# Optimization experiments

Hardware: AMD Instinct MI355X
Metric: run time of the kernel (lower is better)

Reference implementation:

```python
import jax, jax.numpy as jnp
import numpy as np
import math

B, D, K = 16384, 512, 16384  # batch, feature_dim, codebook_size
H, Z = D // 2, D // 4        # encoder hidden (256), code dim (128)
LN_EPS = 1e-5


def _layernorm(x, gamma, beta):
    mu = x.mean(axis=-1, keepdims=True)
    var = ((x - mu) ** 2).mean(axis=-1, keepdims=True)
    return (x - mu) * jax.lax.rsqrt(var + LN_EPS) * gamma + beta


def setup_inputs() -> dict:
    key = jax.random.key(0)
    ks = jax.random.split(key, 8)
    def lin(k, fan_in, fan_out):
        bound = 1.0 / math.sqrt(fan_in)
        kw, kb = jax.random.split(k)
        W = jax.random.uniform(kw, (fan_in, fan_out), jnp.float32, -bound, bound)
        b = jax.random.uniform(kb, (fan_out,), jnp.float32, -bound, bound)
        return W, b
    W1, b1 = lin(ks[0], D, H)
    W2, b2 = lin(ks[1], H, Z)
    W3, b3 = lin(ks[2], Z, H)
    W4, b4 = lin(ks[3], H, D)
    return {
        "features": jax.random.normal(ks[4], (B, D), jnp.float32),
        "W1": W1, "b1": b1,
        "g1": jnp.ones((H,), jnp.float32), "be1": jnp.zeros((H,), jnp.float32),
        "W2": W2, "b2": b2,
        "codebook": jax.random.normal(ks[5], (K, Z), jnp.float32) * 0.1,
        "W3": W3, "b3": b3,
        "g2": jnp.ones((H,), jnp.float32), "be2": jnp.zeros((H,), jnp.float32),
        "W4": W4, "b4": b4,
    }


def reference(features, W1, b1, g1, be1, W2, b2, codebook, W3, b3, g2, be2, W4, b4):
    # encoder: Linear -> LayerNorm -> GELU -> Linear
    h = jax.nn.gelu(_layernorm(features @ W1 + b1, g1, be1), approximate=False)
    encoded = h @ W2 + b2                                    # [B, Z]
    d2 = (jnp.sum(encoded ** 2, axis=-1, keepdims=True)
          + jnp.sum(codebook ** 2, axis=-1)[None, :]
          - 2.0 * encoded @ codebook.T)                      # [B, K]
    distances = jnp.sqrt(jnp.maximum(d2, 0.0))
    quantized_indices = jnp.argmin(distances, axis=-1)       # [B]
    quantized = codebook[quantized_indices]                  # [B, Z]
    # decoder: Linear -> LayerNorm -> GELU -> Linear
    dh = jax.nn.gelu(_layernorm(quantized @ W3 + b3, g2, be2), approximate=False)
    reconstructed = dh @ W4 + b4                             # [B, D]
    reconstruction_error = jnp.mean((reconstructed - features) ** 2, axis=-1)  # [B]
    # MDL bit estimates
    index_bits = math.log2(K)
    scale = reconstruction_error.mean() + 1e-8
    log_prob = -jnp.abs(reconstruction_error) / scale - jnp.log(2.0 * scale)
    error_bits = -log_prob / math.log(2.0)
    total_bits = index_bits + error_bits                     # [B]
    compression_ratio = D * 32.0 / total_bits                # [B]
    return (reconstruction_error, compression_ratio, total_bits, quantized_indices)
```

## Files before the change

### kernel.cpp

```cpp
#include <hip/hip_runtime.h>
#include <math.h>

#define BN 16384
#define DN 512
#define KN 16384
#define HN 256
#define ZN 128

#define EPS_G 0.04f

typedef _Float16 f16x8 __attribute__((ext_vector_type(8)));
typedef _Float16 f16x4 __attribute__((ext_vector_type(4)));
typedef float f32x4 __attribute__((ext_vector_type(4)));

__device__ __forceinline__ unsigned sortkey(float v) {
    unsigned u = __float_as_uint(v);
    return u ^ (0x80000000u | (unsigned)((int)u >> 31));
}
__device__ __forceinline__ float unsortf(unsigned s) {
    unsigned u = (s & 0x80000000u) ? (s ^ 0x80000000u) : ~s;
    return __uint_as_float(u);
}
__device__ __forceinline__ unsigned umin2(unsigned a, unsigned b) { return a < b ? a : b; }
__device__ __forceinline__ unsigned umax2(unsigned a, unsigned b) { return a > b ? a : b; }

__global__ __launch_bounds__(256) void wtrans_kernel(
    const float* __restrict__ W1, const float* __restrict__ W2,
    const float* __restrict__ W3, const float* __restrict__ W4,
    float* __restrict__ Wp1, float* __restrict__ Wp2,
    float* __restrict__ Wp3, float* __restrict__ Wp4)
{
    const int g = blockIdx.x * 256 + threadIdx.x;
    if (g < 131072) {
        const int k = g >> 8, j = g & 255;
        Wp1[((size_t)k * 64 + (j & 63)) * 4 + (j >> 6)] = W1[g];
    } else if (g < 262144) {
        const int i = g - 131072;
        const int k = i >> 9, d = i & 511;
        Wp4[((size_t)k * 128 + (d & 127)) * 4 + (d >> 7)] = W4[i];
    } else if (g < 294912) {
        const int i = g - 262144;
        const int k = i >> 7, j = i & 127;
        Wp2[((size_t)k * 32 + (j & 31)) * 4 + (j >> 5)] = W2[i];
    } else {
        const int i = g - 294912;
        const int k = i >> 8, j = i & 255;
        Wp3[((size_t)k * 64 + (j & 63)) * 4 + (j >> 6)] = W3[i];
    }
}

__global__ __launch_bounds__(256) void enc_kernel(
    const float* __restrict__ feat, const float* __restrict__ Wp1, const float* __restrict__ b1,
    const float* __restrict__ g1, const float* __restrict__ be1,
    const float* __restrict__ Wp2, const float* __restrict__ b2,
    float* __restrict__ encoded, _Float16* __restrict__ xh, _Float16* __restrict__ xl)
{
    __shared__ float xf[16][512];
    __shared__ float hb[16][256];
    const int tid = threadIdx.x;
    const int rbase = blockIdx.x * 16;

    {
        const float4* src = (const float4*)(feat + (size_t)rbase * 512);
        float4* dst = (float4*)&xf[0][0];
        #pragma unroll
        for (int i = 0; i < 8; ++i) dst[tid * 8 + i] = src[tid * 8 + i];
    }
    __syncthreads();

    const int j0 = tid & 63, rg = tid >> 6;
    float acc[4][4];
    #pragma unroll
    for (int c = 0; c < 4; ++c) {
        float bv = b1[c * 64 + j0];
        #pragma unroll
        for (int r = 0; r < 4; ++r) acc[r][c] = bv;
    }
    for (int k = 0; k < 512; k += 4) {
        f32x4 wv[4];
        #pragma unroll
        for (int kk = 0; kk < 4; ++kk)
            wv[kk] = *(const f32x4*)(Wp1 + ((size_t)(k + kk) * 64 + j0) * 4);
        f32x4 xv[4];
        #pragma unroll
        for (int r = 0; r < 4; ++r) xv[r] = *(const f32x4*)&xf[rg * 4 + r][k];
        #pragma unroll
        for (int r = 0; r < 4; ++r)
            #pragma unroll
            for (int c = 0; c < 4; ++c) {
                acc[r][c] = fmaf(xv[r][0], wv[0][c], acc[r][c]);
                acc[r][c] = fmaf(xv[r][1], wv[1][c], acc[r][c]);
                acc[r][c] = fmaf(xv[r][2], wv[2][c], acc[r][c]);
                acc[r][c] = fmaf(xv[r][3], wv[3][c], acc[r][c]);
            }
    }

    float s1[4], s2[4];
    #pragma unroll
    for (int r = 0; r < 4; ++r) {
        s1[r] = acc[r][0] + acc[r][1] + acc[r][2] + acc[r][3];
        s2[r] = acc[r][0] * acc[r][0] + acc[r][1] * acc[r][1]
              + acc[r][2] * acc[r][2] + acc[r][3] * acc[r][3];
    }
    #pragma unroll
    for (int m = 1; m < 64; m <<= 1) {
        #pragma unroll
        for (int r = 0; r < 4; ++r) {
            s1[r] += __shfl_xor(s1[r], m, 64);
            s2[r] += __shfl_xor(s2[r], m, 64);
        }
    }
    {
        float gvv[4], bvv[4];
        #pragma unroll
        for (int c = 0; c < 4; ++c) { gvv[c] = g1[c * 64 + j0]; bvv[c] = be1[c * 64 + j0]; }
        #pragma unroll
        for (int r = 0; r < 4; ++r) {
            float mu = s1[r] * (1.0f / 256.0f);
            float var = fmaxf(s2[r] * (1.0f / 256.0f) - mu * mu, 0.0f);
            float rstd = rsqrtf(var + 1e-5f);
            #pragma unroll
            for (int c = 0; c < 4; ++c) {
                float t = (acc[r][c] - mu) * rstd * gvv[c] + bvv[c];
                hb[rg * 4 + r][c * 64 + j0] = 0.5f * t * (1.0f + erff(t * 0.70710678118654752f));
            }
        }
    }
    __syncthreads();

    const int j02 = tid & 31, rg2 = tid >> 5;
    float a2[2][4];
    #pragma unroll
    for (int c = 0; c < 4; ++c) {
        float bv = b2[c * 32 + j02];
        #pragma unroll
        for (int r = 0; r < 2; ++r) a2[r][c] = bv;
    }
    for (int k = 0; k < 256; k += 4) {
        f32x4 wv[4];
        #pragma unroll
        for (int kk = 0; kk < 4; ++kk)
            wv[kk] = *(const f32x4*)(Wp2 + ((size_t)(k + kk) * 32 + j02) * 4);
        f32x4 hv[2];
        #pragma unroll
        for (int r = 0; r < 2; ++r) hv[r] = *(const f32x4*)&hb[rg2 * 2 + r][k];
        #pragma unroll
        for (int r = 0; r < 2; ++r)
            #pragma unroll
            for (int c = 0; c < 4; ++c) {
                a2[r][c] = fmaf(hv[r][0], wv[0][c], a2[r][c]);
                a2[r][c] = fmaf(hv[r][1], wv[1][c], a2[r][c]);
                a2[r][c] = fmaf(hv[r][2], wv[2][c], a2[r][c]);
                a2[r][c] = fmaf(hv[r][3], wv[3][c], a2[r][c]);
            }
    }
    #pragma unroll
    for (int r = 0; r < 2; ++r) {
        const size_t row = rbase + rg2 * 2 + r;
        #pragma unroll
        for (int c = 0; c < 4; ++c) {
            const size_t idx = row * 128 + c * 32 + j02;
            const float v = a2[r][c];
            encoded[idx] = v;
            _Float16 hh = (_Float16)v;
            xh[idx] = hh;
            xl[idx] = (_Float16)(v - (float)hh);
        }
    }
}

__global__ __launch_bounds__(256) void split_kernel(
    const float* __restrict__ cb, _Float16* __restrict__ cpk, float* __restrict__ cnorm)
{
    const int t = threadIdx.x;
    const int col = blockIdx.x * 8 + (t >> 5);
    const int k0 = (t & 31) * 4;
    float4 v = *(const float4*)(cb + (size_t)col * 128 + k0);
    f16x4 h;
    h.x = (_Float16)v.x;
    h.y = (_Float16)v.y;
    h.z = (_Float16)v.z;
    h.w = (_Float16)v.w;
    const size_t base = (size_t)(col >> 6) * 8192 + (size_t)((col >> 4) & 3) * 2048
                      + (size_t)(k0 >> 3) * 128 + (size_t)(col & 15) * 8 + (k0 & 7);
    *(f16x4*)(cpk + base) = h;

    float s = v.x * v.x + v.y * v.y + v.z * v.z + v.w * v.w;
    #pragma unroll
    for (int m = 1; m < 32; m <<= 1) s += __shfl_xor(s, m, 64);
    if ((t & 31) == 0) cnorm[col] = s;
}

__global__ __launch_bounds__(256, 2) void mfma_dist_kernel(
    const _Float16* __restrict__ xh, const _Float16* __restrict__ xl,
    const _Float16* __restrict__ cpk, const float* __restrict__ cnorm,
    unsigned* __restrict__ gkey)
{
    const int tid = threadIdx.x;
    const int w = tid >> 6, l = tid & 63;
    const int lr = l & 15, lg = l >> 4;
    const int q8 = blockIdx.x & 7;
    const int rb = blockIdx.x >> 3;
    const int rbase = rb * 256 + w * 64;
    const int ctbase = q8 * 32;

    f16x8 xH[4][4], xL[4][4];
    #pragma unroll
    for (int xt = 0; xt < 4; ++xt) {
        const size_t rowoff = (size_t)(rbase + xt * 16 + lr) * 128;
        #pragma unroll
        for (int ks = 0; ks < 4; ++ks) {
            xH[xt][ks] = *(const f16x8*)(xh + rowoff + ks * 32 + lg * 8);
            xL[xt][ks] = *(const f16x8*)(xl + rowoff + ks * 32 + lg * 8);
        }
    }

    for (int t = 0; t < 32; ++t) {
        const int ct = ctbase + t;
        const _Float16* blob = cpk + ((size_t)ct << 13);
        f32x4 acc[4][4];
        #pragma unroll
        for (int c4 = 0; c4 < 4; ++c4)
            #pragma unroll
            for (int xt = 0; xt < 4; ++xt) {
                f32x4 z = {0.0f, 0.0f, 0.0f, 0.0f};
                acc[c4][xt] = z;
            }

        __builtin_amdgcn_s_setprio(1);
        #pragma unroll
        for (int ks = 0; ks < 4; ++ks) {
            f16x8 cH[4];
            #pragma unroll
            for (int c4 = 0; c4 < 4; ++c4) {
                const int off = c4 * 2048 + (ks * 4 + lg) * 128 + lr * 8;
                cH[c4] = *(const f16x8*)(blob + off);
            }
            #pragma unroll
            for (int c4 = 0; c4 < 4; ++c4)
                #pragma unroll
                for (int xt = 0; xt < 4; ++xt) {
                    acc[c4][xt] = __builtin_amdgcn_mfma_f32_16x16x32_f16(cH[c4], xH[xt][ks], acc[c4][xt], 0, 0, 0);
                    acc[c4][xt] = __builtin_amdgcn_mfma_f32_16x16x32_f16(cH[c4], xL[xt][ks], acc[c4][xt], 0, 0, 0);
                }
        }
        __builtin_amdgcn_s_setprio(0);

        float cns[4][4];
        #pragma unroll
        for (int c4 = 0; c4 < 4; ++c4) {
            float4 cv = *(const float4*)(cnorm + ct * 64 + c4 * 16 + lg * 4);
            cns[c4][0] = cv.x; cns[c4][1] = cv.y; cns[c4][2] = cv.z; cns[c4][3] = cv.w;
        }
        const int lg4 = lg * 4;
        #pragma unroll
        for (int xt = 0; xt < 4; ++xt) {
            float v1 = 3.4e38f, v2 = 3.4e38f;
            int i1 = 0;
            #pragma unroll
            for (int c4 = 0; c4 < 4; ++c4)
                #pragma unroll
                for (int reg = 0; reg < 4; ++reg) {
                    float v = fmaf(-2.0f, acc[c4][xt][reg], cns[c4][reg]);
                    int col = c4 * 16 + lg4 + reg;
                    bool cless = v < v1;
                    v2 = fminf(v2, fmaxf(v1, v));
                    v1 = fminf(v1, v);
                    i1 = cless ? col : i1;
                }
            unsigned k1 = (sortkey(v1) & 0xFFFFFF80u) | ((unsigned)i1 << 1);
            unsigned k2 = sortkey(v2) & 0xFFFFFF80u;
            {
                unsigned o1 = (unsigned)__shfl_xor((int)k1, 16, 64);
                unsigned o2 = (unsigned)__shfl_xor((int)k2, 16, 64);
                k2 = umin2(umin2(k2, o2), umax2(k1, o1)); k1 = umin2(k1, o1);
                o1 = (unsigned)__shfl_xor((int)k1, 32, 64);
                o2 = (unsigned)__shfl_xor((int)k2, 32, 64);
                k2 = umin2(umin2(k2, o2), umax2(k1, o1)); k1 = umin2(k1, o1);
            }
            if (lg == 0) {
                float vt1 = unsortf(k1 & 0xFFFFFF80u);
                float vt2 = unsortf(k2);
                unsigned key = k1 | ((vt2 - vt1 <= EPS_G) ? 1u : 0u);
                gkey[(size_t)ct * 16384 + rbase + xt * 16 + lr] = key;
            }
        }
    }
}

#define RCAP 1024
__global__ __launch_bounds__(256) void refine_kernel(
    const float* __restrict__ encoded, const float* __restrict__ cb,
    const float* __restrict__ cnorm, const unsigned* __restrict__ gkey,
    int* __restrict__ idx_ws)
{
    __shared__ unsigned rparts[4][16];
    __shared__ unsigned list[RCAP];
    __shared__ float resV[RCAP];
    __shared__ int resC[RCAP];
    __shared__ float xsm[16][128];
    __shared__ int cnt;
    const int tid = threadIdx.x;
    const int l = tid & 63, wv = tid >> 6;
    const int rbase = blockIdx.x * 16;

    if (tid == 0) cnt = 0;

    unsigned kk[16];
    {
        const unsigned* gp = gkey + (size_t)tid * 16384 + rbase;
        uint4 a0 = *(const uint4*)(gp + 0);
        uint4 a1 = *(const uint4*)(gp + 4);
        uint4 a2 = *(const uint4*)(gp + 8);
        uint4 a3 = *(const uint4*)(gp + 12);
        kk[0] = a0.x; kk[1] = a0.y; kk[2] = a0.z; kk[3] = a0.w;
        kk[4] = a1.x; kk[5] = a1.y; kk[6] = a1.z; kk[7] = a1.w;
        kk[8] = a2.x; kk[9] = a2.y; kk[10] = a2.z; kk[11] = a2.w;
        kk[12] = a3.x; kk[13] = a3.y; kk[14] = a3.z; kk[15] = a3.w;
    }

    #pragma unroll
    for (int r = 0; r < 16; ++r) {
        unsigned m = kk[r];
        #pragma unroll
        for (int mk = 1; mk < 64; mk <<= 1)
            m = umin2(m, (unsigned)__shfl_xor((int)m, mk, 64));
        if (l == 0) rparts[wv][r] = m;
    }
    __syncthreads();

    float rmv[16];
    #pragma unroll
    for (int r = 0; r < 16; ++r) {
        unsigned rm = umin2(umin2(rparts[0][r], rparts[1][r]),
                            umin2(rparts[2][r], rparts[3][r]));
        rmv[r] = unsortf(rm & 0xFFFFFF80u);
    }

    #pragma unroll
    for (int r = 0; r < 16; ++r) {
        float v = unsortf(kk[r] & 0xFFFFFF80u);
        if (v <= rmv[r] + EPS_G) {
            int slot = atomicAdd(&cnt, 1);
            if (slot < RCAP)
                list[slot] = ((unsigned)r << 24) | ((kk[r] & 1u) << 23)
                           | ((unsigned)tid << 6) | ((kk[r] >> 1) & 63u);
        }
    }

    {
        int r = tid >> 4, i = (tid & 15) * 8;
        *(float4*)&xsm[r][i]     = *(const float4*)(encoded + (size_t)(rbase + r) * 128 + i);
        *(float4*)&xsm[r][i + 4] = *(const float4*)(encoded + (size_t)(rbase + r) * 128 + i + 4);
    }
    __syncthreads();

    const int n = min(cnt, RCAP);
    for (int i = wv; i < n; i += 4) {
        unsigned e = list[i];
        const int r = (int)(e >> 24) & 15;
        const int full = (int)(e >> 23) & 1;
        const int c0 = (int)(e & 0x3FFFu);
        const int base = full ? (c0 & ~63) : c0;
        const int ni = full ? 64 : 1;
        float bsv = 3.4e38f; int bc = 0;
        float2 xv = *(const float2*)&xsm[r][l * 2];
        for (int j = 0; j < ni; ++j) {
            const int col = base + j;
            float2 cv = *(const float2*)(cb + (size_t)col * 128 + l * 2);
            float p = fmaf(xv.y, cv.y, xv.x * cv.x);
            #pragma unroll
            for (int mk = 1; mk < 64; mk <<= 1) p += __shfl_xor(p, mk, 64);
            float sc = fmaf(-2.0f, p, cnorm[col]);
            if (sc < bsv) { bsv = sc; bc = col; }
        }
        if (l == 0) { resV[i] = bsv; resC[i] = bc; }
    }
    __syncthreads();

    if (tid < 16) {
        float best = 3.4e38f; int bcol = KN - 1;
        for (int i = 0; i < n; ++i) {
            if ((int)((list[i] >> 24) & 15u) == tid) {
                float v = resV[i]; int c = resC[i];
                if (v < best || (v == best && c < bcol)) { best = v; bcol = c; }
            }
        }
        idx_ws[rbase + tid] = min(max(bcol, 0), KN - 1);
    }
}

__global__ __launch_bounds__(256) void dec_kernel(
    const float* __restrict__ feat, const float* __restrict__ cb,
    const float* __restrict__ Wp3, const float* __restrict__ b3,
    const float* __restrict__ g2, const float* __restrict__ be2,
    const float* __restrict__ Wp4, const float* __restrict__ b4,
    const int* __restrict__ idx_ws,
    float* __restrict__ re_ws, float* __restrict__ sum_ws)
{
    __shared__ float qb[16][128];
    __shared__ float dh[16][256];
    __shared__ float red[4][8];
    __shared__ int idxs[16];
    const int tid = threadIdx.x;
    const int rbase = blockIdx.x * 16;

    if (tid < 16) idxs[tid] = idx_ws[rbase + tid];
    __syncthreads();
    {
        int r = tid >> 4, i = (tid & 15) * 8;
        *(float4*)&qb[r][i]     = *(const float4*)(cb + (size_t)idxs[r] * 128 + i);
        *(float4*)&qb[r][i + 4] = *(const float4*)(cb + (size_t)idxs[r] * 128 + i + 4);
    }
    __syncthreads();

    const int j0 = tid & 63, rg = tid >> 6;
    float acc[4][4];
    #pragma unroll
    for (int c = 0; c < 4; ++c) {
        float bv = b3[c * 64 + j0];
        #pragma unroll
        for (int r = 0; r < 4; ++r) acc[r][c] = bv;
    }
    for (int k = 0; k < 128; k += 4) {
        f32x4 wv[4];
        #pragma unroll
        for (int kk = 0; kk < 4; ++kk)
            wv[kk] = *(const f32x4*)(Wp3 + ((size_t)(k + kk) * 64 + j0) * 4);
        f32x4 qv[4];
        #pragma unroll
        for (int r = 0; r < 4; ++r) qv[r] = *(const f32x4*)&qb[rg * 4 + r][k];
        #pragma unroll
        for (int r = 0; r < 4; ++r)
            #pragma unroll
            for (int c = 0; c < 4; ++c) {
                acc[r][c] = fmaf(qv[r][0], wv[0][c], acc[r][c]);
                acc[r][c] = fmaf(qv[r][1], wv[1][c], acc[r][c]);
                acc[r][c] = fmaf(qv[r][2], wv[2][c], acc[r][c]);
                acc[r][c] = fmaf(qv[r][3], wv[3][c], acc[r][c]);
            }
    }

    float s1[4], s2[4];
    #pragma unroll
    for (int r = 0; r < 4; ++r) {
        s1[r] = acc[r][0] + acc[r][1] + acc[r][2] + acc[r][3];
        s2[r] = acc[r][0] * acc[r][0] + acc[r][1] * acc[r][1]
              + acc[r][2] * acc[r][2] + acc[r][3] * acc[r][3];
    }
    #pragma unroll
    for (int m = 1; m < 64; m <<= 1) {
        #pragma unroll
        for (int r = 0; r < 4; ++r) {
            s1[r] += __shfl_xor(s1[r], m, 64);
            s2[r] += __shfl_xor(s2[r], m, 64);
        }
    }
    {
        float gvv[4], bvv[4];
        #pragma unroll
        for (int c = 0; c < 4; ++c) { gvv[c] = g2[c * 64 + j0]; bvv[c] = be2[c * 64 + j0]; }
        #pragma unroll
        for (int r = 0; r < 4; ++r) {
            float mu = s1[r] * (1.0f / 256.0f);
            float var = fmaxf(s2[r] * (1.0f / 256.0f) - mu * mu, 0.0f);
            float rstd = rsqrtf(var + 1e-5f);
            #pragma unroll
            for (int c = 0; c < 4; ++c) {
                float t = (acc[r][c] - mu) * rstd * gvv[c] + bvv[c];
                dh[rg * 4 + r][c * 64 + j0] = 0.5f * t * (1.0f + erff(t * 0.70710678118654752f));
            }
        }
    }
    __syncthreads();

    const int j04 = tid & 127, rg4 = tid >> 7;
    float a4[8][4];
    #pragma unroll
    for (int c = 0; c < 4; ++c) {
        float bv = b4[c * 128 + j04];
        #pragma unroll
        for (int r = 0; r < 8; ++r) a4[r][c] = bv;
    }
    for (int k = 0; k < 256; k += 4) {
        f32x4 wv[4];
        #pragma unroll
        for (int kk = 0; kk < 4; ++kk)
            wv[kk] = *(const f32x4*)(Wp4 + ((size_t)(k + kk) * 128 + j04) * 4);
        f32x4 hv[8];
        #pragma unroll
        for (int r = 0; r < 8; ++r) hv[r] = *(const f32x4*)&dh[rg4 * 8 + r][k];
        #pragma unroll
        for (int r = 0; r < 8; ++r)
            #pragma unroll
            for (int c = 0; c < 4; ++c) {
                a4[r][c] = fmaf(hv[r][0], wv[0][c], a4[r][c]);
                a4[r][c] = fmaf(hv[r][1], wv[1][c], a4[r][c]);
                a4[r][c] = fmaf(hv[r][2], wv[2][c], a4[r][c]);
                a4[r][c] = fmaf(hv[r][3], wv[3][c], a4[r][c]);
            }
    }
    float e[8];
    #pragma unroll
    for (int r = 0; r < 8; ++r) {
        const float* frow = feat + (size_t)(rbase + rg4 * 8 + r) * 512;
        float d0 = a4[r][0] - frow[j04];
        float d1 = a4[r][1] - frow[128 + j04];
        float d2 = a4[r][2] - frow[256 + j04];
        float d3 = a4[r][3] - frow[384 + j04];
        e[r] = d0 * d0 + d1 * d1 + d2 * d2 + d3 * d3;
    }
    #pragma unroll
    for (int m = 1; m < 64; m <<= 1) {
        #pragma unroll
        for (int r = 0; r < 8; ++r) e[r] += __shfl_xor(e[r], m, 64);
    }
    const int wave = tid >> 6, lane = tid & 63;
    if (lane == 0) {
        #pragma unroll
        for (int r = 0; r < 8; ++r) red[wave][r] = e[r];
    }
    __syncthreads();
    if (tid < 16) {
        float s = (tid < 8) ? (red[0][tid] + red[1][tid])
                            : (red[2][tid - 8] + red[3][tid - 8]);
        s *= (1.0f / 512.0f);
        re_ws[rbase + tid] = s;
        atomicAdd(sum_ws, s);
    }
}

__global__ __launch_bounds__(256) void fin_kernel(
    const float* __restrict__ re_ws, const float* __restrict__ sum_ws,
    const int* __restrict__ idx_ws, float* __restrict__ out)
{
    const int i = blockIdx.x * 256 + threadIdx.x;
    const float scale = (*sum_ws) * (1.0f / 16384.0f) + 1e-8f;
    const float re = re_ws[i];
    const float lp = -fabsf(re) / scale - logf(2.0f * scale);
    const float eb = -lp * 1.4426950408889634f;
    const float tb = 14.0f + eb;
    const float ratio = 16384.0f / tb;
    out[i]             = re;
    out[16384 + i]     = ratio;
    out[2 * 16384 + i] = tb;
    out[3 * 16384 + i] = (float)idx_ws[i];
}

extern "C" void kernel_launch(void* const* d_in, const int* in_sizes, int n_in,
                              void* d_out, int out_size, void* d_ws, size_t ws_size,
                              hipStream_t stream)
{
    const float* feat = (const float*)d_in[0];
    const float* W1   = (const float*)d_in[1];
    const float* b1   = (const float*)d_in[2];
    const float* g1   = (const float*)d_in[3];
    const float* be1  = (const float*)d_in[4];
    const float* W2   = (const float*)d_in[5];
    const float* b2   = (const float*)d_in[6];
    const float* cb   = (const float*)d_in[7];
    const float* W3   = (const float*)d_in[8];
    const float* b3   = (const float*)d_in[9];
    const float* g2   = (const float*)d_in[10];
    const float* be2  = (const float*)d_in[11];
    const float* W4   = (const float*)d_in[12];
    const float* b4   = (const float*)d_in[13];

    char* ws = (char*)d_ws;
    const size_t MB = 1u << 20;
    float*    encoded = (float*)ws;
    _Float16* xh      = (_Float16*)(ws + 8 * MB);
    _Float16* xl      = (_Float16*)(ws + 12 * MB);
    _Float16* cpk     = (_Float16*)(ws + 16 * MB);
    unsigned* gkey    = (unsigned*)(ws + 24 * MB);
    float*    Wp1     = (float*)(ws + 40 * MB);
    float*    Wp2     = (float*)(ws + 40 * MB + (512u << 10));
    float*    Wp3     = (float*)(ws + 40 * MB + (640u << 10));
    float*    Wp4     = (float*)(ws + 40 * MB + (768u << 10));
    float*    cnorm   = (float*)(ws + 41 * MB + (256u << 10));
    float*    re_ws   = (float*)(ws + 41 * MB + (320u << 10));
    int*      idx_ws  = (int*)(ws + 41 * MB + (384u << 10));
    float*    sum_ws  = (float*)(ws + 41 * MB + (448u << 10));

    hipMemsetAsync(sum_ws, 0, sizeof(float), stream);

    hipLaunchKernelGGL(wtrans_kernel, dim3(1280), dim3(256), 0, stream,
                       W1, W2, W3, W4, Wp1, Wp2, Wp3, Wp4);
    hipLaunchKernelGGL(split_kernel, dim3(KN / 8), dim3(256), 0, stream, cb, cpk, cnorm);
    hipLaunchKernelGGL(enc_kernel, dim3(BN / 16), dim3(256), 0, stream,
                       feat, Wp1, b1, g1, be1, Wp2, b2, encoded, xh, xl);
    hipLaunchKernelGGL(mfma_dist_kernel, dim3(64 * 8), dim3(256), 0, stream,
                       xh, xl, cpk, cnorm, gkey);
    hipLaunchKernelGGL(refine_kernel, dim3(BN / 16), dim3(256), 0, stream,
                       encoded, cb, cnorm, gkey, idx_ws);
    hipLaunchKernelGGL(dec_kernel, dim3(BN / 16), dim3(256), 0, stream,
                       feat, cb, Wp3, b3, g2, be2, Wp4, b4,
                       idx_ws, re_ws, sum_ws);
    hipLaunchKernelGGL(fin_kernel, dim3(BN / 256), dim3(256), 0, stream,
                       re_ws, sum_ws, idx_ws, (float*)d_out);
}
```

Before: 486.7 us.

## Store per-group minimum only and rescan whole candidate groups in refine

The distance kernel now keeps only the minimum of each 64-column group per row instead of packed top-2 keys with an index and a closeness flag, which removes the index tracking, second-minimum bookkeeping and sort-key packing from the MFMA epilogue. The refine kernel then rescans every candidate group in full, with each lane computing one column's fp32 dot product from float4 codebook loads, followed by a wave argmin. This makes the hot epilogue cheaper but means refine always does 64 dot products per candidate group rather than a single one when the group's top-2 were well separated.

```diff
diff --git a/kernel.cpp b/kernel.cpp
--- a/kernel.cpp
+++ b/kernel.cpp
@@ -12,17 +12,6 @@
 typedef _Float16 f16x8 __attribute__((ext_vector_type(8)));
 typedef _Float16 f16x4 __attribute__((ext_vector_type(4)));
 typedef float f32x4 __attribute__((ext_vector_type(4)));
-
-__device__ __forceinline__ unsigned sortkey(float v) {
-    unsigned u = __float_as_uint(v);
-    return u ^ (0x80000000u | (unsigned)((int)u >> 31));
-}
-__device__ __forceinline__ float unsortf(unsigned s) {
-    unsigned u = (s & 0x80000000u) ? (s ^ 0x80000000u) : ~s;
-    return __uint_as_float(u);
-}
-__device__ __forceinline__ unsigned umin2(unsigned a, unsigned b) { return a < b ? a : b; }
-__device__ __forceinline__ unsigned umax2(unsigned a, unsigned b) { return a > b ? a : b; }
 
 __global__ __launch_bounds__(256) void wtrans_kernel(
     const float* __restrict__ W1, const float* __restrict__ W2,
@@ -194,7 +183,7 @@
 __global__ __launch_bounds__(256, 2) void mfma_dist_kernel(
     const _Float16* __restrict__ xh, const _Float16* __restrict__ xl,
     const _Float16* __restrict__ cpk, const float* __restrict__ cnorm,
-    unsigned* __restrict__ gkey)
+    float* __restrict__ g_ws)
 {
     const int tid = threadIdx.x;
     const int w = tid >> 6, l = tid & 63;
@@ -252,38 +241,18 @@
             float4 cv = *(const float4*)(cnorm + ct * 64 + c4 * 16 + lg * 4);
             cns[c4][0] = cv.x; cns[c4][1] = cv.y; cns[c4][2] = cv.z; cns[c4][3] = cv.w;
         }
-        const int lg4 = lg * 4;
         #pragma unroll
         for (int xt = 0; xt < 4; ++xt) {
-            float v1 = 3.4e38f, v2 = 3.4e38f;
-            int i1 = 0;
+            float v1 = 3.4e38f;
             #pragma unroll
             for (int c4 = 0; c4 < 4; ++c4)
                 #pragma unroll
-                for (int reg = 0; reg < 4; ++reg) {
-                    float v = fmaf(-2.0f, acc[c4][xt][reg], cns[c4][reg]);
-                    int col = c4 * 16 + lg4 + reg;
-                    bool cless = v < v1;
-                    v2 = fminf(v2, fmaxf(v1, v));
-                    v1 = fminf(v1, v);
-                    i1 = cless ? col : i1;
-                }
-            unsigned k1 = (sortkey(v1) & 0xFFFFFF80u) | ((unsigned)i1 << 1);
-            unsigned k2 = sortkey(v2) & 0xFFFFFF80u;
-            {
-                unsigned o1 = (unsigned)__shfl_xor((int)k1, 16, 64);
-                unsigned o2 = (unsigned)__shfl_xor((int)k2, 16, 64);
-                k2 = umin2(umin2(k2, o2), umax2(k1, o1)); k1 = umin2(k1, o1);
-                o1 = (unsigned)__shfl_xor((int)k1, 32, 64);
-                o2 = (unsigned)__shfl_xor((int)k2, 32, 64);
-                k2 = umin2(umin2(k2, o2), umax2(k1, o1)); k1 = umin2(k1, o1);
-            }
-            if (lg == 0) {
-                float vt1 = unsortf(k1 & 0xFFFFFF80u);
-                float vt2 = unsortf(k2);
-                unsigned key = k1 | ((vt2 - vt1 <= EPS_G) ? 1u : 0u);
-                gkey[(size_t)ct * 16384 + rbase + xt * 16 + lr] = key;
-            }
+                for (int reg = 0; reg < 4; ++reg)
+                    v1 = fminf(v1, fmaf(-2.0f, acc[c4][xt][reg], cns[c4][reg]));
+            v1 = fminf(v1, __shfl_xor(v1, 16, 64));
+            v1 = fminf(v1, __shfl_xor(v1, 32, 64));
+            if (lg == 0)
+                g_ws[(size_t)ct * 16384 + rbase + xt * 16 + lr] = v1;
         }
     }
 }
@@ -291,10 +260,10 @@
 #define RCAP 1024
 __global__ __launch_bounds__(256) void refine_kernel(
     const float* __restrict__ encoded, const float* __restrict__ cb,
-    const float* __restrict__ cnorm, const unsigned* __restrict__ gkey,
+    const float* __restrict__ cnorm, const float* __restrict__ g_ws,
     int* __restrict__ idx_ws)
 {
-    __shared__ unsigned rparts[4][16];
+    __shared__ float rparts[4][16];
     __shared__ unsigned list[RCAP];
     __shared__ float resV[RCAP];
     __shared__ int resC[RCAP];
@@ -306,13 +275,13 @@
 
     if (tid == 0) cnt = 0;
 
-    unsigned kk[16];
+    float kk[16];
     {
-        const unsigned* gp = gkey + (size_t)tid * 16384 + rbase;
-        uint4 a0 = *(const uint4*)(gp + 0);
-        uint4 a1 = *(const uint4*)(gp + 4);
-        uint4 a2 = *(const uint4*)(gp + 8);
-        uint4 a3 = *(const uint4*)(gp + 12);
+        const float* gp = g_ws + (size_t)tid * 16384 + rbase;
+        float4 a0 = *(const float4*)(gp + 0);
+        float4 a1 = *(const float4*)(gp + 4);
+        float4 a2 = *(const float4*)(gp + 8);
+        float4 a3 = *(const float4*)(gp + 12);
         kk[0] = a0.x; kk[1] = a0.y; kk[2] = a0.z; kk[3] = a0.w;
         kk[4] = a1.x; kk[5] = a1.y; kk[6] = a1.z; kk[7] = a1.w;
         kk[8] = a2.x; kk[9] = a2.y; kk[10] = a2.z; kk[11] = a2.w;
@@ -321,30 +290,26 @@
 
     #pragma unroll
     for (int r = 0; r < 16; ++r) {
-        unsigned m = kk[r];
+        float m = kk[r];
         #pragma unroll
         for (int mk = 1; mk < 64; mk <<= 1)
-            m = umin2(m, (unsigned)__shfl_xor((int)m, mk, 64));
+            m = fminf(m, __shfl_xor(m, mk, 64));
         if (l == 0) rparts[wv][r] = m;
     }
     __syncthreads();
 
     float rmv[16];
     #pragma unroll
+    for (int r = 0; r < 16; ++r)
+        rmv[r] = fminf(fminf(rparts[0][r], rparts[1][r]),
+                       fminf(rparts[2][r], rparts[3][r]));
+
+    #pragma unroll
     for (int r = 0; r < 16; ++r) {
-        unsigned rm = umin2(umin2(rparts[0][r], rparts[1][r]),
-                            umin2(rparts[2][r], rparts[3][r]));
-        rmv[r] = unsortf(rm & 0xFFFFFF80u);
-    }
-
-    #pragma unroll
-    for (int r = 0; r < 16; ++r) {
-        float v = unsortf(kk[r] & 0xFFFFFF80u);
-        if (v <= rmv[r] + EPS_G) {
+        if (kk[r] <= rmv[r] + EPS_G) {
             int slot = atomicAdd(&cnt, 1);
             if (slot < RCAP)
-                list[slot] = ((unsigned)r << 24) | ((kk[r] & 1u) << 23)
-                           | ((unsigned)tid << 6) | ((kk[r] >> 1) & 63u);
+                list[slot] = ((unsigned)r << 8) | (unsigned)tid;
         }
     }
 
@@ -357,31 +322,38 @@
 
     const int n = min(cnt, RCAP);
     for (int i = wv; i < n; i += 4) {
-        unsigned e = list[i];
-        const int r = (int)(e >> 24) & 15;
-        const int full = (int)(e >> 23) & 1;
-        const int c0 = (int)(e & 0x3FFFu);
-        const int base = full ? (c0 & ~63) : c0;
-        const int ni = full ? 64 : 1;
-        float bsv = 3.4e38f; int bc = 0;
-        float2 xv = *(const float2*)&xsm[r][l * 2];
-        for (int j = 0; j < ni; ++j) {
-            const int col = base + j;
-            float2 cv = *(const float2*)(cb + (size_t)col * 128 + l * 2);
-            float p = fmaf(xv.y, cv.y, xv.x * cv.x);
-            #pragma unroll
-            for (int mk = 1; mk < 64; mk <<= 1) p += __shfl_xor(p, mk, 64);
-            float sc = fmaf(-2.0f, p, cnorm[col]);
-            if (sc < bsv) { bsv = sc; bc = col; }
-        }
-        if (l == 0) { resV[i] = bsv; resC[i] = bc; }
+        const unsigned e = list[i];
+        const int r = (int)(e >> 8);
+        const int grp = (int)(e & 255u);
+        const int col = grp * 64 + l;
+        const float4* cp = (const float4*)(cb + (size_t)col * 128);
+        const float* xr = &xsm[r][0];
+        float a0 = 0.0f, a1 = 0.0f, a2 = 0.0f, a3 = 0.0f;
+        #pragma unroll 8
+        for (int z = 0; z < 32; ++z) {
+            float4 c4v = cp[z];
+            a0 = fmaf(xr[4 * z + 0], c4v.x, a0);
+            a1 = fmaf(xr[4 * z + 1], c4v.y, a1);
+            a2 = fmaf(xr[4 * z + 2], c4v.z, a2);
+            a3 = fmaf(xr[4 * z + 3], c4v.w, a3);
+        }
+        float dot = (a0 + a1) + (a2 + a3);
+        float bv = fmaf(-2.0f, dot, cnorm[col]);
+        int bc = col;
+        #pragma unroll
+        for (int mk = 1; mk < 64; mk <<= 1) {
+            float ov = __shfl_xor(bv, mk, 64);
+            int oi = __shfl_xor(bc, mk, 64);
+            if (ov < bv || (ov == bv && oi < bc)) { bv = ov; bc = oi; }
+        }
+        if (l == 0) { resV[i] = bv; resC[i] = bc; }
     }
     __syncthreads();
 
     if (tid < 16) {
         float best = 3.4e38f; int bcol = KN - 1;
         for (int i = 0; i < n; ++i) {
-            if ((int)((list[i] >> 24) & 15u) == tid) {
+            if ((int)(list[i] >> 8) == tid) {
                 float v = resV[i]; int c = resC[i];
                 if (v < best || (v == best && c < bcol)) { best = v; bcol = c; }
             }
@@ -572,7 +544,7 @@
     _Float16* xh      = (_Float16*)(ws + 8 * MB);
     _Float16* xl      = (_Float16*)(ws + 12 * MB);
     _Float16* cpk     = (_Float16*)(ws + 16 * MB);
-    unsigned* gkey    = (unsigned*)(ws + 24 * MB);
+    float*    g_ws    = (float*)(ws + 24 * MB);
     float*    Wp1     = (float*)(ws + 40 * MB);
     float*    Wp2     = (float*)(ws + 40 * MB + (512u << 10));
     float*    Wp3     = (float*)(ws + 40 * MB + (640u << 10));
@@ -590,9 +562,9 @@
     hipLaunchKernelGGL(enc_kernel, dim3(BN / 16), dim3(256), 0, stream,
                        feat, Wp1, b1, g1, be1, Wp2, b2, encoded, xh, xl);
     hipLaunchKernelGGL(mfma_dist_kernel, dim3(64 * 8), dim3(256), 0, stream,
-                       xh, xl, cpk, cnorm, gkey);
+                       xh, xl, cpk, cnorm, g_ws);
     hipLaunchKernelGGL(refine_kernel, dim3(BN / 16), dim3(256), 0, stream,
-                       encoded, cb, cnorm, gkey, idx_ws);
+                       encoded, cb, cnorm, g_ws, idx_ws);
     hipLaunchKernelGGL(dec_kernel, dim3(BN / 16), dim3(256), 0, stream,
                        feat, cb, Wp3, b3, g2, be2, Wp4, b4,
                        idx_ws, re_ws, sum_ws);
```

Result: slower. 515.1 us (+5.8%).
